# Kernel optimization log

Hardware: AMD Instinct MI355X
Metric: run time of the kernel (lower is better)

## Reference

```python
import jax, jax.numpy as jnp
import numpy as np

OUT_F, IN_F = 8192, 4096
TOKENS = 512


def _unpack_int2_to_ternary(packed, alpha, dtype):
    # packed: [out_f, in_f//4] ints 0..255; 4 two-bit codes per byte.
    # code 0 -> -1, code 2 -> +1, codes 1/3 -> 0; then scale by per-row alpha.
    shifts = jnp.arange(4, dtype=packed.dtype) * 2  # [0,2,4,6]
    two_bit = (packed[:, :, None] >> shifts[None, None, :]) & 3  # [out_f, in_f//4, 4]
    two_bit = two_bit.reshape(packed.shape[0], -1)  # [out_f, in_f]
    sign = jnp.where(two_bit == 2, 1.0, jnp.where(two_bit == 0, -1.0, 0.0)).astype(dtype)
    return sign * alpha.astype(dtype)[:, None]


def setup_inputs() -> dict:
    key = jax.random.key(0)
    k1, k2, k3, k4 = jax.random.split(key, 4)
    x = jax.random.normal(k1, (TOKENS, IN_F), dtype=jnp.float32)
    weight_int2 = jax.random.randint(k2, (OUT_F, IN_F // 4), 0, 256, dtype=jnp.int32)
    alpha = jax.random.uniform(k3, (OUT_F,), dtype=jnp.float32, minval=0.01, maxval=0.05)
    bias = jax.random.normal(k4, (OUT_F,), dtype=jnp.float32) * 0.01
    return {"x": x, "weight_int2": weight_int2, "alpha": alpha, "bias": bias}


def reference(x, weight_int2, alpha, bias):
    W = _unpack_int2_to_ternary(weight_int2, alpha, x.dtype)  # [out_f, in_f]
    out = x @ W.T  # [tokens, out_f]
    return out + bias
```

## Files before the change

kernel.cpp:

```cpp
#include <hip/hip_runtime.h>
#include <hip/hip_bf16.h>

typedef unsigned int u32;
typedef unsigned short u16;

#define TOKENS 512
#define OUT_F  8192
#define IN_F   4096
#define KPACK  (IN_F / 4)

#define TM 128
#define TN 64
#define BK 64
#define NSTEP (IN_F / BK)

typedef __attribute__((ext_vector_type(8))) short bf16x8;
typedef __attribute__((ext_vector_type(4))) float f32x4;

__device__ __forceinline__ u32 pack_bf16x2(float a, float b) {
    __hip_bfloat162 h = __float22bfloat162_rn(make_float2(a, b));
    union { __hip_bfloat162 h2; u32 u; } cvt;
    cvt.h2 = h;
    return cvt.u;
}

__device__ __forceinline__ void decode4(u32 w, u32& lo, u32& hi) {
    u32 t = (w & 0xFFu) * 0x4001u;
    u32 u = t >> 4;
    u32 nt = ~t;
    u32 nu = ~u;
    lo = ((nt & 0x10001u) * 0x3F80u) | ((nt & 0x20002u) << 14);
    hi = ((nu & 0x10001u) * 0x3F80u) | ((nu & 0x20002u) << 14);
}

__device__ __forceinline__ void async_ld16(const void* g, void* l) {
    __builtin_amdgcn_global_load_lds(
        (const __attribute__((address_space(1))) u32*)g,
        (__attribute__((address_space(3))) u32*)l, 16, 0, 0);
}

__global__ __launch_bounds__(256) void convert_x(const float* __restrict__ X,
                                                 u16* __restrict__ Xb) {
    int i = (blockIdx.x * 256 + threadIdx.x) * 8;
    float4 a = *(const float4*)(X + i);
    float4 b = *(const float4*)(X + i + 4);
    uint4 q;
    q.x = pack_bf16x2(a.x, a.y);
    q.y = pack_bf16x2(a.z, a.w);
    q.z = pack_bf16x2(b.x, b.y);
    q.w = pack_bf16x2(b.z, b.w);
    *(uint4*)(Xb + i) = q;
}


template <bool PRE>
__global__ __launch_bounds__(256, 2) void ternary_gemm(
    const float* __restrict__ Xf,
    const u16* __restrict__ Xb,
    const u32* __restrict__ W2,
    const float* __restrict__ alpha,
    const float* __restrict__ bias,
    float* __restrict__ Out)
{
    __shared__ u16 As[2][TM * BK];
    __shared__ u16 Bs[2][TN * BK];

    const int tid  = threadIdx.x;
    const int lane = tid & 63;
    const int wave = tid >> 6;
    const int quad = lane >> 4;
    const int lr   = lane & 15;

    const int n0 = blockIdx.x * TN;
    const int m0 = blockIdx.y * TM;

    const int wm = (wave >> 1) * 64;
    const int wn = (wave & 1) * 32;

    f32x4 acc[4][2];
#pragma unroll
    for (int i = 0; i < 4; ++i)
#pragma unroll
        for (int j = 0; j < 2; ++j)
            acc[i][j] = (f32x4){0.f, 0.f, 0.f, 0.f};

    const int brow = tid >> 2;
    const int h    = tid & 3;
    const int bp   = brow & 7;
    const int be   = (2 * h) ^ (bp & 6);
    const u32* w2row = W2 + (size_t)(n0 + brow) * KPACK + be * 2;

    auto load_w2 = [&](int ks) -> uint4 {
        return *(const uint4*)(w2row + (ks >> 2));
    };

    auto stage_b = [&](const uint4& w, int buf) {
        u32 a0, a1, b0, b1, c0, c1, d0, d1;
        decode4(w.x, a0, a1);
        decode4(w.y, b0, b1);
        decode4(w.z, c0, c1);
        decode4(w.w, d0, d1);
        uint4 qa = {a0, a1, b0, b1};
        uint4 qb = {c0, c1, d0, d1};
        int po = bp & 1;
        *(uint4*)&Bs[buf][brow * BK + (2 * h + po) * 8]       = qa;
        *(uint4*)&Bs[buf][brow * BK + (2 * h + (po ^ 1)) * 8] = qb;
    };

    auto stage_a_dma = [&](int ks, int buf) {
#pragma unroll
        for (int i = 0; i < 4; ++i) {
            int rbase = wave * 32 + i * 8;
            int row = rbase + (lane >> 3);
            int c = (lane & 7) ^ (row & 7);
            const u16* g = Xb + (size_t)(m0 + row) * IN_F + ks + c * 8;
            async_ld16(g, &As[buf][rbase * BK]);
        }
    };

    auto stage_a_f32 = [&](int ks, int buf) {
#pragma unroll
        for (int i = 0; i < 4; ++i) {
            int id = i * 256 + tid;
            int row = id >> 3, s = id & 7;
            int c = s ^ (row & 7);
            const float* p = Xf + (size_t)(m0 + row) * IN_F + ks + c * 8;
            float4 fa = *(const float4*)p;
            float4 fb = *(const float4*)(p + 4);
            uint4 q;
            q.x = pack_bf16x2(fa.x, fa.y);
            q.y = pack_bf16x2(fa.z, fa.w);
            q.z = pack_bf16x2(fb.x, fb.y);
            q.w = pack_bf16x2(fb.z, fb.w);
            *(uint4*)&As[buf][row * BK + s * 8] = q;
        }
    };

    auto compute = [&](int buf) {
        bf16x8 af[4][2], bfv[2][2];
#pragma unroll
        for (int kk = 0; kk < 2; ++kk) {
            int s = (kk * 4 + quad) ^ (lr & 7);
#pragma unroll
            for (int mt = 0; mt < 4; ++mt)
                af[mt][kk] = *(const bf16x8*)&As[buf][(wm + mt * 16 + lr) * BK + s * 8];
#pragma unroll
            for (int nt = 0; nt < 2; ++nt)
                bfv[nt][kk] = *(const bf16x8*)&Bs[buf][(wn + nt * 16 + lr) * BK + s * 8];
        }
#pragma unroll
        for (int kk = 0; kk < 2; ++kk)
#pragma unroll
            for (int mt = 0; mt < 4; ++mt)
#pragma unroll
                for (int nt = 0; nt < 2; ++nt)
                    acc[mt][nt] = __builtin_amdgcn_mfma_f32_16x16x32_bf16(
                        af[mt][kk], bfv[nt][kk], acc[mt][nt], 0, 0, 0);
    };

    uint4 wcur = load_w2(0);
    if (PRE) stage_a_dma(0, 0); else stage_a_f32(0, 0);
    stage_b(wcur, 0);
    uint4 wnext = load_w2(BK);
    __syncthreads();

    for (int s = 0; s < NSTEP; ++s) {
        int buf = s & 1;
        if (s + 1 < NSTEP) {
            if (PRE) stage_a_dma((s + 1) * BK, buf ^ 1);
            else     stage_a_f32((s + 1) * BK, buf ^ 1);
            stage_b(wnext, buf ^ 1);
        }
        if (s + 2 < NSTEP) wnext = load_w2((s + 2) * BK);
        compute(buf);
        __syncthreads();
    }

#pragma unroll
    for (int nt = 0; nt < 2; ++nt) {
        int ncol = n0 + wn + nt * 16 + lr;
        float av = alpha[ncol];
        float bv = bias[ncol];
#pragma unroll
        for (int mt = 0; mt < 4; ++mt) {
            int mbase = m0 + wm + mt * 16 + quad * 4;
#pragma unroll
            for (int r = 0; r < 4; ++r) {
                Out[(size_t)(mbase + r) * OUT_F + ncol] = acc[mt][nt][r] * av + bv;
            }
        }
    }
}

extern "C" void kernel_launch(void* const* d_in, const int* in_sizes, int n_in,
                              void* d_out, int out_size, void* d_ws, size_t ws_size,
                              hipStream_t stream) {
    const float* x = (const float*)d_in[0];
    const u32* w2 = (const u32*)d_in[1];
    const float* alpha = (const float*)d_in[2];
    const float* bias  = (const float*)d_in[3];
    float* out = (float*)d_out;

    dim3 grid(OUT_F / TN, TOKENS / TM);

    const size_t need = (size_t)TOKENS * IN_F * sizeof(u16);
    if (ws_size >= need) {
        u16* xb = (u16*)d_ws;
        convert_x<<<(TOKENS * IN_F) / (256 * 8), 256, 0, stream>>>(x, xb);
        ternary_gemm<true><<<grid, 256, 0, stream>>>(x, xb, w2, alpha, bias, out);
    } else {
        ternary_gemm<false><<<grid, 256, 0, stream>>>(x, nullptr, w2, alpha, bias, out);
    }
}
```

Measured before the change: 147.3 us.

## Repack ternary weights into MFMA fragment order and decode in registers

Adds a repack kernel that compresses the int32-per-byte weights into dense 2-bit codes laid out in the exact per-lane MFMA fragment order. The GEMM then loads one uint2 per lane per K step and decodes B fragments in registers, dropping the B shared-memory buffer and its LDS writes and reads. Launch bounds are raised to 4 blocks per CU to use the freed LDS. The cost is an extra repack pass over the full weight tensor on every call, plus a workspace requirement for the packed weights.

```diff
diff --git a/kernel.cpp b/kernel.cpp
--- a/kernel.cpp
+++ b/kernel.cpp
@@ -31,6 +31,15 @@
     u32 nu = ~u;
     lo = ((nt & 0x10001u) * 0x3F80u) | ((nt & 0x20002u) << 14);
     hi = ((nu & 0x10001u) * 0x3F80u) | ((nu & 0x20002u) << 14);
+}
+
+__device__ __forceinline__ bf16x8 decode_frag(u32 hw) {
+    u32 d0, d1, d2, d3;
+    decode4(hw, d0, d1);
+    decode4(hw >> 8, d2, d3);
+    union { bf16x8 v; u32 u[4]; } c;
+    c.u[0] = d0; c.u[1] = d1; c.u[2] = d2; c.u[3] = d3;
+    return c.v;
 }
 
 __device__ __forceinline__ void async_ld16(const void* g, void* l) {
@@ -52,18 +61,55 @@
     *(uint4*)(Xb + i) = q;
 }
 
-
-template <bool PRE>
-__global__ __launch_bounds__(256, 2) void ternary_gemm(
+__global__ __launch_bounds__(256) void repack_w(const u32* __restrict__ W2,
+                                                uint2* __restrict__ W4) {
+    __shared__ u32 staged[32 * 256];
+    const int ng = blockIdx.x;
+    const int t  = threadIdx.x;
+
+    {
+        int r = t >> 3, c8 = t & 7;
+        size_t base = (size_t)(ng * 32 + r) * KPACK + c8 * 128;
+#pragma unroll
+        for (int i = 0; i < 32; ++i) {
+            uint4 w = *(const uint4*)(W2 + base + 4 * i);
+            staged[r * 256 + c8 * 32 + i] =
+                (w.x & 0xFFu) | ((w.y & 0xFFu) << 8) |
+                ((w.z & 0xFFu) << 16) | ((w.w & 0xFFu) << 24);
+        }
+    }
+    __syncthreads();
+    {
+        const u16* sp = (const u16*)staged;
+#pragma unroll
+        for (int j = 0; j < 16; ++j) {
+            int u = t + 256 * j;
+            int S = u >> 6, l = u & 63;
+            int lr = l & 15, quad = l >> 4;
+            u32 lo0 = sp[lr * 512 + S * 8 + quad];
+            u32 hi0 = sp[lr * 512 + S * 8 + 4 + quad];
+            u32 lo1 = sp[(lr + 16) * 512 + S * 8 + quad];
+            u32 hi1 = sp[(lr + 16) * 512 + S * 8 + 4 + quad];
+            uint2 o;
+            o.x = lo0 | (hi0 << 16);
+            o.y = lo1 | (hi1 << 16);
+            W4[((size_t)ng * NSTEP + S) * 64 + l] = o;
+        }
+    }
+}
+
+
+template <bool PRE, bool PACKED>
+__global__ __launch_bounds__(256, 4) void ternary_gemm(
     const float* __restrict__ Xf,
     const u16* __restrict__ Xb,
     const u32* __restrict__ W2,
+    const uint2* __restrict__ W4,
     const float* __restrict__ alpha,
     const float* __restrict__ bias,
     float* __restrict__ Out)
 {
     __shared__ u16 As[2][TM * BK];
-    __shared__ u16 Bs[2][TN * BK];
 
     const int tid  = threadIdx.x;
     const int lane = tid & 63;
@@ -73,9 +119,9 @@
 
     const int n0 = blockIdx.x * TN;
     const int m0 = blockIdx.y * TM;
-
     const int wm = (wave >> 1) * 64;
     const int wn = (wave & 1) * 32;
+    const int ng32 = (n0 + wn) >> 5;
 
     f32x4 acc[4][2];
 #pragma unroll
@@ -83,29 +129,6 @@
 #pragma unroll
         for (int j = 0; j < 2; ++j)
             acc[i][j] = (f32x4){0.f, 0.f, 0.f, 0.f};
-
-    const int brow = tid >> 2;
-    const int h    = tid & 3;
-    const int bp   = brow & 7;
-    const int be   = (2 * h) ^ (bp & 6);
-    const u32* w2row = W2 + (size_t)(n0 + brow) * KPACK + be * 2;
-
-    auto load_w2 = [&](int ks) -> uint4 {
-        return *(const uint4*)(w2row + (ks >> 2));
-    };
-
-    auto stage_b = [&](const uint4& w, int buf) {
-        u32 a0, a1, b0, b1, c0, c1, d0, d1;
-        decode4(w.x, a0, a1);
-        decode4(w.y, b0, b1);
-        decode4(w.z, c0, c1);
-        decode4(w.w, d0, d1);
-        uint4 qa = {a0, a1, b0, b1};
-        uint4 qb = {c0, c1, d0, d1};
-        int po = bp & 1;
-        *(uint4*)&Bs[buf][brow * BK + (2 * h + po) * 8]       = qa;
-        *(uint4*)&Bs[buf][brow * BK + (2 * h + (po ^ 1)) * 8] = qb;
-    };
 
     auto stage_a_dma = [&](int ks, int buf) {
 #pragma unroll
@@ -136,32 +159,44 @@
         }
     };
 
-    auto compute = [&](int buf) {
-        bf16x8 af[4][2], bfv[2][2];
+    auto load_w = [&](int s) -> uint2 {
+        if (PACKED) {
+            return W4[((size_t)ng32 * NSTEP + s) * 64 + lane];
+        } else {
+            const u32* r0 = W2 + (size_t)(n0 + wn + lr) * KPACK + s * 16 + quad * 2;
+            const u32* r1 = W2 + (size_t)(n0 + wn + 16 + lr) * KPACK + s * 16 + quad * 2;
+            uint2 a0 = *(const uint2*)r0, b0 = *(const uint2*)(r0 + 8);
+            uint2 a1 = *(const uint2*)r1, b1 = *(const uint2*)(r1 + 8);
+            uint2 w;
+            w.x = (a0.x & 0xFFu) | ((a0.y & 0xFFu) << 8) |
+                  ((b0.x & 0xFFu) << 16) | ((b0.y & 0xFFu) << 24);
+            w.y = (a1.x & 0xFFu) | ((a1.y & 0xFFu) << 8) |
+                  ((b1.x & 0xFFu) << 16) | ((b1.y & 0xFFu) << 24);
+            return w;
+        }
+    };
+
+    auto compute = [&](int buf, uint2 wreg) {
 #pragma unroll
         for (int kk = 0; kk < 2; ++kk) {
-            int s = (kk * 4 + quad) ^ (lr & 7);
+            int sl = (kk * 4 + quad) ^ (lr & 7);
+            bf16x8 af[4];
 #pragma unroll
             for (int mt = 0; mt < 4; ++mt)
-                af[mt][kk] = *(const bf16x8*)&As[buf][(wm + mt * 16 + lr) * BK + s * 8];
-#pragma unroll
-            for (int nt = 0; nt < 2; ++nt)
-                bfv[nt][kk] = *(const bf16x8*)&Bs[buf][(wn + nt * 16 + lr) * BK + s * 8];
-        }
-#pragma unroll
-        for (int kk = 0; kk < 2; ++kk)
-#pragma unroll
-            for (int mt = 0; mt < 4; ++mt)
-#pragma unroll
-                for (int nt = 0; nt < 2; ++nt)
-                    acc[mt][nt] = __builtin_amdgcn_mfma_f32_16x16x32_bf16(
-                        af[mt][kk], bfv[nt][kk], acc[mt][nt], 0, 0, 0);
-    };
-
-    uint4 wcur = load_w2(0);
+                af[mt] = *(const bf16x8*)&As[buf][(wm + mt * 16 + lr) * BK + sl * 8];
+            bf16x8 b0 = decode_frag(kk ? (wreg.x >> 16) : (wreg.x & 0xFFFFu));
+            bf16x8 b1 = decode_frag(kk ? (wreg.y >> 16) : (wreg.y & 0xFFFFu));
+#pragma unroll
+            for (int mt = 0; mt < 4; ++mt) {
+                acc[mt][0] = __builtin_amdgcn_mfma_f32_16x16x32_bf16(af[mt], b0, acc[mt][0], 0, 0, 0);
+                acc[mt][1] = __builtin_amdgcn_mfma_f32_16x16x32_bf16(af[mt], b1, acc[mt][1], 0, 0, 0);
+            }
+        }
+    };
+
+    uint2 wcur = load_w(0);
+    uint2 wnext = load_w(1);
     if (PRE) stage_a_dma(0, 0); else stage_a_f32(0, 0);
-    stage_b(wcur, 0);
-    uint4 wnext = load_w2(BK);
     __syncthreads();
 
     for (int s = 0; s < NSTEP; ++s) {
@@ -169,10 +204,11 @@
         if (s + 1 < NSTEP) {
             if (PRE) stage_a_dma((s + 1) * BK, buf ^ 1);
             else     stage_a_f32((s + 1) * BK, buf ^ 1);
-            stage_b(wnext, buf ^ 1);
-        }
-        if (s + 2 < NSTEP) wnext = load_w2((s + 2) * BK);
-        compute(buf);
+        }
+        uint2 wnn = (s + 2 < NSTEP) ? load_w(s + 2) : make_uint2(0, 0);
+        compute(buf, wcur);
+        wcur = wnext;
+        wnext = wnn;
         __syncthreads();
     }
 
@@ -203,12 +239,20 @@
 
     dim3 grid(OUT_F / TN, TOKENS / TM);
 
-    const size_t need = (size_t)TOKENS * IN_F * sizeof(u16);
-    if (ws_size >= need) {
+    const size_t xb_bytes = (size_t)TOKENS * IN_F * sizeof(u16);
+    const size_t w4_bytes = (size_t)OUT_F * IN_F / 4;
+
+    if (ws_size >= xb_bytes + w4_bytes) {
+        u16* xb = (u16*)d_ws;
+        uint2* w4 = (uint2*)((char*)d_ws + xb_bytes);
+        convert_x<<<(TOKENS * IN_F) / (256 * 8), 256, 0, stream>>>(x, xb);
+        repack_w<<<OUT_F / 32, 256, 0, stream>>>(w2, w4);
+        ternary_gemm<true, true><<<grid, 256, 0, stream>>>(x, xb, w2, w4, alpha, bias, out);
+    } else if (ws_size >= xb_bytes) {
         u16* xb = (u16*)d_ws;
         convert_x<<<(TOKENS * IN_F) / (256 * 8), 256, 0, stream>>>(x, xb);
-        ternary_gemm<true><<<grid, 256, 0, stream>>>(x, xb, w2, alpha, bias, out);
+        ternary_gemm<true, false><<<grid, 256, 0, stream>>>(x, xb, w2, nullptr, alpha, bias, out);
     } else {
-        ternary_gemm<false><<<grid, 256, 0, stream>>>(x, nullptr, w2, alpha, bias, out);
-    }
-}
+        ternary_gemm<false, false><<<grid, 256, 0, stream>>>(x, nullptr, w2, nullptr, alpha, bias, out);
+    }
+}
```

Result: faster. 144.1 us (-2.2%).
